# Performance work log

Measured on AMD Instinct MI355X. Metric: run time of the kernel, lower is better.

The kernel has to match this reference:

```python
import jax, jax.numpy as jnp
import numpy as np
import math

PHI = (1 + math.sqrt(5)) / 2
VOCAB = 50257
EMBED_DIM = 1024
NUM_WINDINGS = 8
EPS = 1e-5


def _generate_coprimes(n):
    coprimes = [1, 2]
    while len(coprimes) < n:
        nxt = int(coprimes[-1] * PHI) + 1
        while any(math.gcd(nxt, c) > 1 for c in coprimes):
            nxt += 1
        coprimes.append(nxt)
    return coprimes[:n]


def setup_inputs() -> dict:
    key = jax.random.key(0)
    k1, k2, k3 = jax.random.split(key, 3)
    B, S = 8, 4096
    x = jax.random.randint(k1, (B, S), 0, VOCAB, dtype=jnp.int64)
    windings = jnp.asarray(_generate_coprimes(NUM_WINDINGS), dtype=jnp.float32)
    win_dim = 2 * NUM_WINDINGS
    # nn.Linear default init: U(-1/sqrt(fan_in), 1/sqrt(fan_in))
    bound = 1.0 / math.sqrt(win_dim)
    proj_w = jax.random.uniform(k2, (EMBED_DIM, win_dim), jnp.float32, -bound, bound)
    proj_b = jax.random.uniform(k3, (EMBED_DIM,), jnp.float32, -bound, bound)
    gamma = jnp.ones((EMBED_DIM,), jnp.float32)
    beta = jnp.zeros((EMBED_DIM,), jnp.float32)
    return {"x": x, "windings": windings, "proj_w": proj_w, "proj_b": proj_b,
            "gamma": gamma, "beta": beta}


def reference(x, windings, proj_w, proj_b, gamma, beta):
    # t in [0,1): fractional position on the torus
    t = x.astype(jnp.float32) / VOCAB                      # (B, S)
    angle = (2.0 * jnp.pi) * t[..., None] * windings       # (B, S, W)
    # torch loop appends cos, sin per winding -> interleaved [cos0,sin0,cos1,sin1,...]
    feats = jnp.stack([jnp.cos(angle), jnp.sin(angle)], axis=-1)  # (B, S, W, 2)
    feats = feats.reshape(*angle.shape[:-1], 2 * windings.shape[0])  # (B, S, 2W)
    emb = jnp.einsum('bsf,df->bsd', feats, proj_w) + proj_b  # (B, S, D)
    # SyntonicNorm: LayerNorm-style normalization over embed_dim with affine params
    mu = jnp.mean(emb, axis=-1, keepdims=True)
    var = jnp.mean(jnp.square(emb - mu), axis=-1, keepdims=True)
    normed = (emb - mu) * jax.lax.rsqrt(var + EPS)
    return normed * gamma + beta
```

## Files before the change

### kernel.cpp

```cpp
#include <hip/hip_runtime.h>
#include <math.h>


#define TWO_PI 6.28318530717958647692f
#define INV_VOCAB (1.0f / 50257.0f)
#define INV_D (1.0f / 1024.0f)

typedef float f32x4 __attribute__((ext_vector_type(4)));

__global__ __launch_bounds__(256, 4) void wind_fused(const int* __restrict__ x,
                                                     const float* __restrict__ winds,
                                                     const float* __restrict__ pw,
                                                     const float* __restrict__ pb,
                                                     const float* __restrict__ gamma,
                                                     const float* __restrict__ beta,
                                                     float* __restrict__ out) {
  __shared__ __align__(16) float feat[16][16];
  __shared__ float red[2][4][4][2];

  const int tid = threadIdx.x;
  const int wave = tid >> 6;
  const int lane = tid & 63;
  const int base = blockIdx.x * 16;
  const int d0 = tid << 2;

  float4 wreg[4][4];
#pragma unroll
  for (int r = 0; r < 4; ++r)
#pragma unroll
    for (int c = 0; c < 4; ++c)
      wreg[r][c] = reinterpret_cast<const float4*>(pw)[(d0 + r) * 4 + c];
  const float4 pbv = reinterpret_cast<const float4*>(pb)[tid];

  {
    const int rl = tid >> 4;
    const int j = tid & 15;
    const float tf = (float)x[base + rl] * INV_VOCAB;
    float s, c;
    sincosf(TWO_PI * tf * winds[j >> 1], &s, &c);
    feat[rl][j] = (j & 1) ? s : c;
  }
  __syncthreads();

  const float4 gv = reinterpret_cast<const float4*>(gamma)[tid];
  const float4 bv = reinterpret_cast<const float4*>(beta)[tid];

#pragma unroll
  for (int h = 0; h < 4; ++h) {
    float er[4][4];
    float sr[4], qr[4];

#pragma unroll
    for (int r = 0; r < 4; ++r) {
      const int rr = h * 4 + r;
      const float4 F0 = *reinterpret_cast<const float4*>(&feat[rr][0]);
      const float4 F1 = *reinterpret_cast<const float4*>(&feat[rr][4]);
      const float4 F2 = *reinterpret_cast<const float4*>(&feat[rr][8]);
      const float4 F3 = *reinterpret_cast<const float4*>(&feat[rr][12]);
#pragma unroll
      for (int k = 0; k < 4; ++k) {
        float a = (k == 0) ? pbv.x : (k == 1) ? pbv.y : (k == 2) ? pbv.z : pbv.w;
        a = fmaf(wreg[k][0].x, F0.x, a);
        a = fmaf(wreg[k][0].y, F0.y, a);
        a = fmaf(wreg[k][0].z, F0.z, a);
        a = fmaf(wreg[k][0].w, F0.w, a);
        a = fmaf(wreg[k][1].x, F1.x, a);
        a = fmaf(wreg[k][1].y, F1.y, a);
        a = fmaf(wreg[k][1].z, F1.z, a);
        a = fmaf(wreg[k][1].w, F1.w, a);
        a = fmaf(wreg[k][2].x, F2.x, a);
        a = fmaf(wreg[k][2].y, F2.y, a);
        a = fmaf(wreg[k][2].z, F2.z, a);
        a = fmaf(wreg[k][2].w, F2.w, a);
        a = fmaf(wreg[k][3].x, F3.x, a);
        a = fmaf(wreg[k][3].y, F3.y, a);
        a = fmaf(wreg[k][3].z, F3.z, a);
        a = fmaf(wreg[k][3].w, F3.w, a);
        er[r][k] = a;
      }
      sr[r] = (er[r][0] + er[r][1]) + (er[r][2] + er[r][3]);
      float q = er[r][0] * er[r][0];
      q = fmaf(er[r][1], er[r][1], q);
      q = fmaf(er[r][2], er[r][2], q);
      q = fmaf(er[r][3], er[r][3], q);
      qr[r] = q;
    }

#pragma unroll
    for (int r = 0; r < 4; ++r) {
#pragma unroll
      for (int off = 1; off < 64; off <<= 1) {
        sr[r] += __shfl_xor(sr[r], off);
        qr[r] += __shfl_xor(qr[r], off);
      }
    }
    if (lane == 0) {
#pragma unroll
      for (int r = 0; r < 4; ++r) {
        red[h & 1][wave][r][0] = sr[r];
        red[h & 1][wave][r][1] = qr[r];
      }
    }
    __syncthreads();

    float* o = out + (size_t)(base + h * 4) * 1024 + d0;
#pragma unroll
    for (int r = 0; r < 4; ++r) {
      const float s = (red[h & 1][0][r][0] + red[h & 1][1][r][0]) +
                      (red[h & 1][2][r][0] + red[h & 1][3][r][0]);
      const float q = (red[h & 1][0][r][1] + red[h & 1][1][r][1]) +
                      (red[h & 1][2][r][1] + red[h & 1][3][r][1]);
      const float mu = s * INV_D;
      const float var = fmaf(q, INV_D, -mu * mu);
      const float rs = rsqrtf(var + 1e-5f);
      const float s0 = gv.x * rs, s1 = gv.y * rs, s2 = gv.z * rs, s3 = gv.w * rs;
      f32x4 res;
      res.x = fmaf(er[r][0], s0, fmaf(-mu, s0, bv.x));
      res.y = fmaf(er[r][1], s1, fmaf(-mu, s1, bv.y));
      res.z = fmaf(er[r][2], s2, fmaf(-mu, s2, bv.z));
      res.w = fmaf(er[r][3], s3, fmaf(-mu, s3, bv.w));
      __builtin_nontemporal_store(res, reinterpret_cast<f32x4*>(o + (size_t)r * 1024));
    }
  }
}

extern "C" void kernel_launch(void* const* d_in, const int* in_sizes, int n_in,
                              void* d_out, int out_size, void* d_ws, size_t ws_size,
                              hipStream_t stream) {
  const int* x = (const int*)d_in[0];
  const float* winds = (const float*)d_in[1];
  const float* pw = (const float*)d_in[2];
  const float* pb = (const float*)d_in[3];
  const float* gamma = (const float*)d_in[4];
  const float* beta = (const float*)d_in[5];
  float* out = (float*)d_out;

  const int rows = in_sizes[0];
  wind_fused<<<rows / 16, 256, 0, stream>>>(x, winds, pw, pb, gamma, beta, out);
}
```

Before: 50.43 us.

## Process 64 rows per block to amortize weight loads and drop nontemporal stores

Each 256-thread block now handles 64 token rows instead of 16. The per-thread projection weights, bias, gamma and beta registers are loaded once and reused across 16 row-groups, with feature computation spread over four passes. The shared feature tile is padded to 20 columns, launch_bounds is removed, and output stores become regular stores instead of nontemporal ones. Launching 4x fewer blocks cuts redundant weight loads but may leave too few waves per CU to hide latency on the store-bound output write, and cache behaviour changes without the nontemporal hint.

```diff
diff --git a/kernel.cpp b/kernel.cpp
--- a/kernel.cpp
+++ b/kernel.cpp
@@ -5,58 +5,58 @@
 #define TWO_PI 6.28318530717958647692f
 #define INV_VOCAB (1.0f / 50257.0f)
 #define INV_D (1.0f / 1024.0f)
+#define ROWS_PB 64
 
 typedef float f32x4 __attribute__((ext_vector_type(4)));
 
-__global__ __launch_bounds__(256, 4) void wind_fused(const int* __restrict__ x,
-                                                     const float* __restrict__ winds,
-                                                     const float* __restrict__ pw,
-                                                     const float* __restrict__ pb,
-                                                     const float* __restrict__ gamma,
-                                                     const float* __restrict__ beta,
-                                                     float* __restrict__ out) {
-  __shared__ __align__(16) float feat[16][16];
+__global__ void wind_fused(const int* __restrict__ x,
+                           const float* __restrict__ winds,
+                           const float* __restrict__ pw,
+                           const float* __restrict__ pb,
+                           const float* __restrict__ gamma,
+                           const float* __restrict__ beta,
+                           float* __restrict__ out) {
+  __shared__ __align__(16) float feat[ROWS_PB][20];
   __shared__ float red[2][4][4][2];
 
   const int tid = threadIdx.x;
   const int wave = tid >> 6;
   const int lane = tid & 63;
-  const int base = blockIdx.x * 16;
-  const int d0 = tid << 2;
+  const int row0 = blockIdx.x * ROWS_PB;
 
   float4 wreg[4][4];
 #pragma unroll
   for (int r = 0; r < 4; ++r)
 #pragma unroll
     for (int c = 0; c < 4; ++c)
-      wreg[r][c] = reinterpret_cast<const float4*>(pw)[(d0 + r) * 4 + c];
+      wreg[r][c] = reinterpret_cast<const float4*>(pw)[(tid * 4 + r) * 4 + c];
   const float4 pbv = reinterpret_cast<const float4*>(pb)[tid];
-
-  {
-    const int rl = tid >> 4;
-    const int j = tid & 15;
-    const float tf = (float)x[base + rl] * INV_VOCAB;
-    float s, c;
-    sincosf(TWO_PI * tf * winds[j >> 1], &s, &c);
-    feat[rl][j] = (j & 1) ? s : c;
-  }
-  __syncthreads();
-
   const float4 gv = reinterpret_cast<const float4*>(gamma)[tid];
   const float4 bv = reinterpret_cast<const float4*>(beta)[tid];
 
 #pragma unroll
-  for (int h = 0; h < 4; ++h) {
+  for (int s = 0; s < 4; ++s) {
+    const int slot = tid + s * 256;
+    const int r = slot >> 4, jj = slot & 15;
+    const float tf = (float)x[row0 + r] * INV_VOCAB;
+    float sn, cs;
+    sincosf(TWO_PI * tf * winds[jj >> 1], &sn, &cs);
+    feat[r][jj] = (jj & 1) ? sn : cs;
+  }
+  __syncthreads();
+
+#pragma unroll 2
+  for (int h = 0; h < 16; ++h) {
     float er[4][4];
     float sr[4], qr[4];
 
 #pragma unroll
     for (int r = 0; r < 4; ++r) {
       const int rr = h * 4 + r;
-      const float4 F0 = *reinterpret_cast<const float4*>(&feat[rr][0]);
-      const float4 F1 = *reinterpret_cast<const float4*>(&feat[rr][4]);
-      const float4 F2 = *reinterpret_cast<const float4*>(&feat[rr][8]);
-      const float4 F3 = *reinterpret_cast<const float4*>(&feat[rr][12]);
+      const f32x4 F0 = *reinterpret_cast<const f32x4*>(&feat[rr][0]);
+      const f32x4 F1 = *reinterpret_cast<const f32x4*>(&feat[rr][4]);
+      const f32x4 F2 = *reinterpret_cast<const f32x4*>(&feat[rr][8]);
+      const f32x4 F3 = *reinterpret_cast<const f32x4*>(&feat[rr][12]);
 #pragma unroll
       for (int k = 0; k < 4; ++k) {
         float a = (k == 0) ? pbv.x : (k == 1) ? pbv.y : (k == 2) ? pbv.z : pbv.w;
@@ -103,7 +103,7 @@
     }
     __syncthreads();
 
-    float* o = out + (size_t)(base + h * 4) * 1024 + d0;
+    float* o = out + (size_t)(row0 + h * 4) * 1024 + tid * 4;
 #pragma unroll
     for (int r = 0; r < 4; ++r) {
       const float s = (red[h & 1][0][r][0] + red[h & 1][1][r][0]) +
@@ -119,7 +119,7 @@
       res.y = fmaf(er[r][1], s1, fmaf(-mu, s1, bv.y));
       res.z = fmaf(er[r][2], s2, fmaf(-mu, s2, bv.z));
       res.w = fmaf(er[r][3], s3, fmaf(-mu, s3, bv.w));
-      __builtin_nontemporal_store(res, reinterpret_cast<f32x4*>(o + (size_t)r * 1024));
+      *reinterpret_cast<f32x4*>(o + (size_t)r * 1024) = res;
     }
   }
 }
@@ -136,5 +136,5 @@
   float* out = (float*)d_out;
 
   const int rows = in_sizes[0];
-  wind_fused<<<rows / 16, 256, 0, stream>>>(x, winds, pw, pb, gamma, beta, out);
+  wind_fused<<<rows / ROWS_PB, 256, 0, stream>>>(x, winds, pw, pb, gamma, beta, out);
 }
```

Result: faster. 47.22 us (-6.4%).
